# Kernel tuning notes

Measured on AMD Instinct MI355X. Metric: run time of the kernel, lower is better.

## Reference

```python
import jax, jax.numpy as jnp
import numpy as np

H = 0.5
EPS = 1e-08


def setup_inputs() -> dict:
    key = jax.random.key(0)
    k1, k2, k3 = jax.random.split(key, 3)
    B, in_dim, n_rules, out_dim = 16384, 64, 128, 32
    X = jax.random.normal(k1, (B, in_dim), dtype=jnp.float32)
    centers = jax.random.normal(k2, (in_dim, n_rules), dtype=jnp.float32)
    sigmas = jnp.ones((in_dim, n_rules), dtype=jnp.float32)
    W = jax.random.normal(k3, (out_dim, (in_dim + 1) * n_rules), dtype=jnp.float32) * 0.02
    b = jnp.zeros((out_dim,), dtype=jnp.float32)
    return {"X": X, "centers": centers, "sigmas": sigmas, "W": W, "b": b}


def reference(X, centers, sigmas, W, b):
    # HTSK firing levels: mean-style scaled Gaussian log-memberships summed over in_dim
    scale = H / sigmas ** 2 + EPS                      # [in_dim, n_rules]
    diff = X[:, :, None] - centers[None, :, :]          # [B, in_dim, n_rules]
    logits = jnp.sum(-(diff ** 2) * scale, axis=1)      # [B, n_rules]
    frs = jax.nn.softmax(logits, axis=1)                # [B, n_rules]
    B = X.shape[0]
    # order=1 consequent input: rule-major outer product, then raw firing levels
    xr = (frs[:, :, None] * X[:, None, :]).reshape(B, -1)  # [B, n_rules*in_dim]
    Z = jnp.concatenate([xr, frs], axis=1)               # [B, n_rules*(in_dim+1)]
    output = Z @ W.T + b                                 # [B, out_dim]
    return output, frs
```

## Files before the change

### kernel.cpp

```cpp
#include <hip/hip_runtime.h>


#define H_CONST 0.5f
#define EPS_CONST 1e-8f
#define NROWS 16384
#define NRULES 128
#define WCOLS 8320

typedef _Float16 half8 __attribute__((ext_vector_type(8)));
typedef float floatx4 __attribute__((ext_vector_type(4)));

#define MFMA16(a, b, c) __builtin_amdgcn_mfma_f32_16x16x32_f16((a), (b), (c), 0, 0, 0)

#define WFRAG_OFF 0
#define W0FRAG_OFF 262144
#define BMAT_OFF   (262144 + 4096)
#define KVEC_BYTE_OFF 630784
#define WS_BYTES_NEEDED (630784 + 512)

__global__ __launch_bounds__(256) void prep_kernel(
    const float* __restrict__ centers, const float* __restrict__ sigmas,
    const float* __restrict__ W, _Float16* __restrict__ wsh)
{
    __shared__ float sBuf[32 * 68];
    const int t = threadIdx.x;
    const int b = blockIdx.x;

    if (b < 128) {
        const int r = b;
        {
            int o = t >> 3, seg = t & 7;
            const float* g = W + o * WCOLS + r * 64 + seg * 8;
            floatx4 a = *(const floatx4*)g;
            floatx4 c = *(const floatx4*)(g + 4);
            *(floatx4*)(sBuf + o * 68 + seg * 8) = a;
            *(floatx4*)(sBuf + o * 68 + seg * 8 + 4) = c;
        }
        __syncthreads();
        {
            int L = t & 63, nt = (t >> 6) & 1, s = t >> 7;
            int o = nt * 16 + (L & 15);
            int ib = s * 32 + ((L >> 4) & 3) * 8;
            floatx4 fa = *(const floatx4*)(sBuf + o * 68 + ib);
            floatx4 fb = *(const floatx4*)(sBuf + o * 68 + ib + 4);
            half8 h;
#pragma unroll
            for (int k = 0; k < 8; ++k) h[k] = (_Float16)((k < 4) ? fa[k & 3] : fb[k & 3]);
            *(half8*)(wsh + WFRAG_OFF + r * 2048 + t * 8) = h;
        }
    } else if (b < 136) {
        const int nt = b - 128;
        float* sS = sBuf;
        float* sC = sBuf + 1088;
        {
            int i = t >> 2, c0 = (t & 3) * 4;
            floatx4 sg4 = *(const floatx4*)(sigmas + i * NRULES + nt * 16 + c0);
            floatx4 ct4 = *(const floatx4*)(centers + i * NRULES + nt * 16 + c0);
#pragma unroll
            for (int k = 0; k < 4; ++k) { sS[i * 17 + c0 + k] = sg4[k]; sC[i * 17 + c0 + k] = ct4[k]; }
        }
        __syncthreads();
#pragma unroll
        for (int kk = 0; kk < 3; ++kk) {
            int unit = t + kk * 256;
            int s = unit >> 6, L = unit & 63;
            int q = (L >> 4) & 3, nl = L & 15;
            int g = s >> 1;
            int i0 = (s & 1) * 32 + q * 8;
            half8 h;
#pragma unroll
            for (int j = 0; j < 8; ++j) {
                int i = i0 + j;
                float sg = sS[i * 17 + nl];
                float S = H_CONST / (sg * sg) + EPS_CONST;
                float c = sC[i * 17 + nl];
                float CS2 = 2.0f * c * S;
                _Float16 v;
                if (g == 0 || g == 2) v = -(_Float16)S;
                else if (g == 1) { _Float16 sh = (_Float16)S; v = -(_Float16)(S - (float)sh); }
                else if (g == 3 || g == 5) v = (_Float16)CS2;
                else { _Float16 ch = (_Float16)CS2; v = (_Float16)(CS2 - (float)ch); }
                h[j] = v;
            }
            *(half8*)(wsh + BMAT_OFF + ((s * 8 + nt) * 64 + L) * 8) = h;
        }
    } else {
#pragma unroll
        for (int kk = 0; kk < 2; ++kk) {
            int unit = t + kk * 256;
            int s = unit >> 7, nt = (unit >> 6) & 1, L = unit & 63;
            int q = (L >> 4) & 3;
            int o = nt * 16 + (L & 15);
            half8 h;
#pragma unroll
            for (int j = 0; j < 8; ++j) {
                int r = s * 32 + q * 8 + j;
                h[j] = (_Float16)W[o * WCOLS + 8192 + r];
            }
            *(half8*)(wsh + W0FRAG_OFF + ((s * 2 + nt) * 64 + L) * 8) = h;
        }
    }
}

__global__ __launch_bounds__(128) void prep_kvec(
    const float* __restrict__ centers, const float* __restrict__ sigmas,
    float* __restrict__ kvec)
{
    int r = threadIdx.x;
    float acc = 0.f;
#pragma unroll 8
    for (int i = 0; i < 64; ++i) {
        float sg = sigmas[i * NRULES + r];
        float S = H_CONST / (sg * sg) + EPS_CONST;
        float c = centers[i * NRULES + r];
        acc += c * c * S;
    }
    kvec[r] = acc;
}

__global__ __launch_bounds__(256) void main_fused(
    const float* __restrict__ X, const float* __restrict__ bias,
    const _Float16* __restrict__ wsh, const float* __restrict__ kvec,
    float* __restrict__ out, float* __restrict__ frs_out)
{
    __shared__ _Float16 sXh[32 * 64];
    __shared__ _Float16 sXl[32 * 64];
    __shared__ _Float16 sX2h[32 * 64];
    __shared__ _Float16 sX2l[32 * 64];
    __shared__ _Float16 sF[32 * 136];
    __shared__ float sU[4608];

    const int t = threadIdx.x;
    const int w = t >> 6;
    const int L = t & 63;
    const int m = L & 15;
    const int q = L >> 4;
    const int row0 = blockIdx.x * 32;

    {
        int row = t >> 3, uc = t & 7;
        const float* gx = X + (row0 + row) * 64 + uc * 8;
        floatx4 xa = *(const floatx4*)gx;
        floatx4 xb = *(const floatx4*)(gx + 4);
        int base = row * 64 + (uc ^ (row & 7)) * 8;
        half8 vh, vl, v2h, v2l;
#pragma unroll
        for (int k = 0; k < 8; ++k) {
            float x = (k < 4) ? xa[k & 3] : xb[k & 3];
            _Float16 xh = (_Float16)x;
            _Float16 xl2 = (_Float16)(x - (float)xh);
            float x2 = x * x;
            _Float16 x2h = (_Float16)x2;
            _Float16 x2l = (_Float16)(x2 - (float)x2h);
            vh[k] = xh; vl[k] = xl2; v2h[k] = x2h; v2l[k] = x2l;
        }
        *(half8*)(sXh + base) = vh;
        *(half8*)(sXl + base) = vl;
        *(half8*)(sX2h + base) = v2h;
        *(half8*)(sX2l + base) = v2l;
    }
    __syncthreads();

    floatx4 lacc[2][2];
#pragma unroll
    for (int mt = 0; mt < 2; ++mt)
#pragma unroll
        for (int n = 0; n < 2; ++n) lacc[mt][n] = (floatx4){0.f, 0.f, 0.f, 0.f};

    const _Float16* Bm = wsh + BMAT_OFF;
#pragma unroll
    for (int s = 0; s < 12; ++s) {
        const _Float16* arr = (s < 4) ? sX2h : (s < 6) ? sX2l : (s < 10) ? sXh : sXl;
        int phys = (((s & 1) << 2) | q) ^ (m & 7);
        half8 b0 = *(const half8*)(Bm + ((s * 8 + 2 * w + 0) * 64 + L) * 8);
        half8 b1 = *(const half8*)(Bm + ((s * 8 + 2 * w + 1) * 64 + L) * 8);
#pragma unroll
        for (int mt = 0; mt < 2; ++mt) {
            half8 a = *(const half8*)(arr + (mt * 16 + m) * 64 + phys * 8);
            lacc[mt][0] = MFMA16(a, b0, lacc[mt][0]);
            lacc[mt][1] = MFMA16(a, b1, lacc[mt][1]);
        }
    }
    float kv0 = kvec[(2 * w + 0) * 16 + m];
    float kv1 = kvec[(2 * w + 1) * 16 + m];

#pragma unroll
    for (int mt = 0; mt < 2; ++mt)
#pragma unroll
        for (int ntl = 0; ntl < 2; ++ntl)
#pragma unroll
            for (int reg = 0; reg < 4; ++reg) {
                int rl = mt * 16 + q * 4 + reg;
                int col = (2 * w + ntl) * 16 + m;
                sU[rl * 132 + col] = lacc[mt][ntl][reg] - (ntl ? kv1 : kv0);
            }
    __syncthreads();

    {
        int row = t >> 3, l8 = t & 7;
        int base = row * 132 + l8 * 16;
        float v[16];
        float mx = -1e30f;
#pragma unroll
        for (int k = 0; k < 16; ++k) { v[k] = sU[base + k]; mx = fmaxf(mx, v[k]); }
        mx = fmaxf(mx, __shfl_xor(mx, 1));
        mx = fmaxf(mx, __shfl_xor(mx, 2));
        mx = fmaxf(mx, __shfl_xor(mx, 4));
        float sum = 0.f;
#pragma unroll
        for (int k = 0; k < 16; ++k) { v[k] = __expf(v[k] - mx); sum += v[k]; }
        sum += __shfl_xor(sum, 1);
        sum += __shfl_xor(sum, 2);
        sum += __shfl_xor(sum, 4);
        float inv = 1.0f / sum;
        float* gf = frs_out + (row0 + row) * 128 + l8 * 16;
        half8 h0, h1;
#pragma unroll
        for (int c = 0; c < 4; ++c) {
            floatx4 o4;
#pragma unroll
            for (int k = 0; k < 4; ++k) {
                float f = v[c * 4 + k] * inv;
                o4[k] = f;
                if (c < 2) h0[c * 4 + k] = (_Float16)f; else h1[(c - 2) * 4 + k] = (_Float16)f;
            }
            *(floatx4*)(gf + c * 4) = o4;
        }
        *(half8*)(sF + row * 136 + l8 * 16) = h0;
        *(half8*)(sF + row * 136 + l8 * 16 + 8) = h1;
    }
    __syncthreads();

    const int rq = w;
    const int r0 = rq * 32;
    const _Float16* Wf = wsh + WFRAG_OFF;
    const _Float16* W0f = wsh + W0FRAG_OFF;

#define LDW(r, slot) (*(const half8*)(Wf + (r) * 2048 + ((slot) * 64 + L) * 8))

    half8 xf[2][2];
#pragma unroll
    for (int mt = 0; mt < 2; ++mt)
#pragma unroll
        for (int s = 0; s < 2; ++s) {
            int phys = ((s << 2) | q) ^ (m & 7);
            xf[mt][s] = *(const half8*)(sXh + (mt * 16 + m) * 64 + phys * 8);
        }

    floatx4 oacc[2][2];
#pragma unroll
    for (int mt = 0; mt < 2; ++mt)
#pragma unroll
        for (int n = 0; n < 2; ++n) oacc[mt][n] = (floatx4){0.f, 0.f, 0.f, 0.f};

    half8 b00 = LDW(r0, 0), b01 = LDW(r0, 1), b10 = LDW(r0, 2), b11 = LDW(r0, 3);

#pragma unroll
    for (int rg = 0; rg < 4; ++rg) {
        half8 fv0 = *(const half8*)(sF + (0 * 16 + m) * 136 + r0 + rg * 8);
        half8 fv1 = *(const half8*)(sF + (1 * 16 + m) * 136 + r0 + rg * 8);
#pragma unroll
        for (int rr2 = 0; rr2 < 8; ++rr2) {
            half8 c00 = b00, c01 = b01, c10 = b10, c11 = b11;
            if (rg * 8 + rr2 < 31) {
                int rn = r0 + rg * 8 + rr2 + 1;
                b00 = LDW(rn, 0); b01 = LDW(rn, 1); b10 = LDW(rn, 2); b11 = LDW(rn, 3);
            }
            _Float16 f0 = fv0[rr2], f1 = fv1[rr2];
            half8 fs0, fs1;
#pragma unroll
            for (int k = 0; k < 8; ++k) { fs0[k] = f0; fs1[k] = f1; }
            half8 a00 = fs0 * xf[0][0];
            half8 a01 = fs0 * xf[0][1];
            half8 a10 = fs1 * xf[1][0];
            half8 a11 = fs1 * xf[1][1];
            oacc[0][0] = MFMA16(a00, c00, oacc[0][0]);
            oacc[0][0] = MFMA16(a01, c10, oacc[0][0]);
            oacc[0][1] = MFMA16(a00, c01, oacc[0][1]);
            oacc[0][1] = MFMA16(a01, c11, oacc[0][1]);
            oacc[1][0] = MFMA16(a10, c00, oacc[1][0]);
            oacc[1][0] = MFMA16(a11, c10, oacc[1][0]);
            oacc[1][1] = MFMA16(a10, c01, oacc[1][1]);
            oacc[1][1] = MFMA16(a11, c11, oacc[1][1]);
        }
    }

    {
        half8 wb0 = *(const half8*)(W0f + ((rq * 2 + 0) * 64 + L) * 8);
        half8 wb1 = *(const half8*)(W0f + ((rq * 2 + 1) * 64 + L) * 8);
#pragma unroll
        for (int mt = 0; mt < 2; ++mt) {
            half8 a = *(const half8*)(sF + (mt * 16 + m) * 136 + rq * 32 + q * 8);
            oacc[mt][0] = MFMA16(a, wb0, oacc[mt][0]);
            oacc[mt][1] = MFMA16(a, wb1, oacc[mt][1]);
        }
    }

#pragma unroll
    for (int mt = 0; mt < 2; ++mt)
#pragma unroll
        for (int ntl = 0; ntl < 2; ++ntl)
#pragma unroll
            for (int reg = 0; reg < 4; ++reg)
                sU[w * 1152 + (mt * 16 + q * 4 + reg) * 36 + ntl * 16 + m] = oacc[mt][ntl][reg];
    __syncthreads();

    {
        int row = t >> 3, col0 = (t & 7) * 4;
        floatx4 acc = *(const floatx4*)(sU + 0 * 1152 + row * 36 + col0);
        acc += *(const floatx4*)(sU + 1 * 1152 + row * 36 + col0);
        acc += *(const floatx4*)(sU + 2 * 1152 + row * 36 + col0);
        acc += *(const floatx4*)(sU + 3 * 1152 + row * 36 + col0);
        acc += *(const floatx4*)(bias + col0);
        *(floatx4*)(out + (row0 + row) * 32 + col0) = acc;
    }
#undef LDW
}

extern "C" void kernel_launch(void* const* d_in, const int* in_sizes, int n_in,
                              void* d_out, int out_size, void* d_ws, size_t ws_size,
                              hipStream_t stream) {
    const float* X = (const float*)d_in[0];
    const float* centers = (const float*)d_in[1];
    const float* sigmas = (const float*)d_in[2];
    const float* W = (const float*)d_in[3];
    const float* b = (const float*)d_in[4];
    float* outp = (float*)d_out;
    float* frs_out = outp + NROWS * 32;
    if (ws_size < (size_t)WS_BYTES_NEEDED) return;
    _Float16* wsh = (_Float16*)d_ws;
    float* kvec = (float*)((char*)d_ws + KVEC_BYTE_OFF);

    prep_kernel<<<137, 256, 0, stream>>>(centers, sigmas, W, wsh);
    prep_kvec<<<1, 128, 0, stream>>>(centers, sigmas, kvec);
    main_fused<<<NROWS / 32, 256, 0, stream>>>(X, b, wsh, kvec, outp, frs_out);
}
```

Baseline: 91.04 us.

## Merge kvec prep into prep kernel and prefetch weight fragments earlier

```diff
diff --git a/kernel.cpp b/kernel.cpp
--- a/kernel.cpp
+++ b/kernel.cpp
@@ -20,7 +20,7 @@
 
 __global__ __launch_bounds__(256) void prep_kernel(
     const float* __restrict__ centers, const float* __restrict__ sigmas,
-    const float* __restrict__ W, _Float16* __restrict__ wsh)
+    const float* __restrict__ W, _Float16* __restrict__ wsh, float* __restrict__ kvec)
 {
     __shared__ float sBuf[32 * 68];
     const int t = threadIdx.x;
@@ -99,23 +99,19 @@
             }
             *(half8*)(wsh + W0FRAG_OFF + ((s * 2 + nt) * 64 + L) * 8) = h;
         }
-    }
-}
-
-__global__ __launch_bounds__(128) void prep_kvec(
-    const float* __restrict__ centers, const float* __restrict__ sigmas,
-    float* __restrict__ kvec)
-{
-    int r = threadIdx.x;
-    float acc = 0.f;
+        if (t < 128) {
+            int r = t;
+            float acc = 0.f;
 #pragma unroll 8
-    for (int i = 0; i < 64; ++i) {
-        float sg = sigmas[i * NRULES + r];
-        float S = H_CONST / (sg * sg) + EPS_CONST;
-        float c = centers[i * NRULES + r];
-        acc += c * c * S;
-    }
-    kvec[r] = acc;
+            for (int i = 0; i < 64; ++i) {
+                float sg = sigmas[i * NRULES + r];
+                float S = H_CONST / (sg * sg) + EPS_CONST;
+                float c = centers[i * NRULES + r];
+                acc += c * c * S;
+            }
+            kvec[r] = acc;
+        }
+    }
 }
 
 __global__ __launch_bounds__(256) void main_fused(
@@ -137,6 +133,16 @@
     const int q = L >> 4;
     const int row0 = blockIdx.x * 32;
 
+    const _Float16* Bm = wsh + BMAT_OFF;
+    half8 Bv[12][2];
+#pragma unroll
+    for (int s = 0; s < 12; ++s) {
+        Bv[s][0] = *(const half8*)(Bm + ((s * 8 + 2 * w + 0) * 64 + L) * 8);
+        Bv[s][1] = *(const half8*)(Bm + ((s * 8 + 2 * w + 1) * 64 + L) * 8);
+    }
+    float kv0 = kvec[(2 * w + 0) * 16 + m];
+    float kv1 = kvec[(2 * w + 1) * 16 + m];
+
     {
         int row = t >> 3, uc = t & 7;
         const float* gx = X + (row0 + row) * 64 + uc * 8;
@@ -167,22 +173,17 @@
 #pragma unroll
         for (int n = 0; n < 2; ++n) lacc[mt][n] = (floatx4){0.f, 0.f, 0.f, 0.f};
 
-    const _Float16* Bm = wsh + BMAT_OFF;
 #pragma unroll
     for (int s = 0; s < 12; ++s) {
         const _Float16* arr = (s < 4) ? sX2h : (s < 6) ? sX2l : (s < 10) ? sXh : sXl;
         int phys = (((s & 1) << 2) | q) ^ (m & 7);
-        half8 b0 = *(const half8*)(Bm + ((s * 8 + 2 * w + 0) * 64 + L) * 8);
-        half8 b1 = *(const half8*)(Bm + ((s * 8 + 2 * w + 1) * 64 + L) * 8);
 #pragma unroll
         for (int mt = 0; mt < 2; ++mt) {
             half8 a = *(const half8*)(arr + (mt * 16 + m) * 64 + phys * 8);
-            lacc[mt][0] = MFMA16(a, b0, lacc[mt][0]);
-            lacc[mt][1] = MFMA16(a, b1, lacc[mt][1]);
-        }
-    }
-    float kv0 = kvec[(2 * w + 0) * 16 + m];
-    float kv1 = kvec[(2 * w + 1) * 16 + m];
+            lacc[mt][0] = MFMA16(a, Bv[s][0], lacc[mt][0]);
+            lacc[mt][1] = MFMA16(a, Bv[s][1], lacc[mt][1]);
+        }
+    }
 
 #pragma unroll
     for (int mt = 0; mt < 2; ++mt)
@@ -194,6 +195,24 @@
                 int col = (2 * w + ntl) * 16 + m;
                 sU[rl * 132 + col] = lacc[mt][ntl][reg] - (ntl ? kv1 : kv0);
             }
+
+    const int rq = w;
+    const int r0 = rq * 32;
+    const _Float16* Wf = wsh + WFRAG_OFF;
+    const _Float16* W0f = wsh + W0FRAG_OFF;
+#define LDW(r, slot) (*(const half8*)(Wf + (r) * 2048 + ((slot) * 64 + L) * 8))
+
+    half8 ring[4][4];
+#pragma unroll
+    for (int p = 0; p < 4; ++p) {
+        ring[p][0] = LDW(r0 + p, 0);
+        ring[p][1] = LDW(r0 + p, 1);
+        ring[p][2] = LDW(r0 + p, 2);
+        ring[p][3] = LDW(r0 + p, 3);
+    }
+    half8 wb0 = *(const half8*)(W0f + ((rq * 2 + 0) * 64 + L) * 8);
+    half8 wb1 = *(const half8*)(W0f + ((rq * 2 + 1) * 64 + L) * 8);
+
     __syncthreads();
 
     {
@@ -231,13 +250,6 @@
     }
     __syncthreads();
 
-    const int rq = w;
-    const int r0 = rq * 32;
-    const _Float16* Wf = wsh + WFRAG_OFF;
-    const _Float16* W0f = wsh + W0FRAG_OFF;
-
-#define LDW(r, slot) (*(const half8*)(Wf + (r) * 2048 + ((slot) * 64 + L) * 8))
-
     half8 xf[2][2];
 #pragma unroll
     for (int mt = 0; mt < 2; ++mt)
@@ -253,18 +265,22 @@
 #pragma unroll
         for (int n = 0; n < 2; ++n) oacc[mt][n] = (floatx4){0.f, 0.f, 0.f, 0.f};
 
-    half8 b00 = LDW(r0, 0), b01 = LDW(r0, 1), b10 = LDW(r0, 2), b11 = LDW(r0, 3);
-
 #pragma unroll
     for (int rg = 0; rg < 4; ++rg) {
         half8 fv0 = *(const half8*)(sF + (0 * 16 + m) * 136 + r0 + rg * 8);
         half8 fv1 = *(const half8*)(sF + (1 * 16 + m) * 136 + r0 + rg * 8);
 #pragma unroll
         for (int rr2 = 0; rr2 < 8; ++rr2) {
-            half8 c00 = b00, c01 = b01, c10 = b10, c11 = b11;
-            if (rg * 8 + rr2 < 31) {
-                int rn = r0 + rg * 8 + rr2 + 1;
-                b00 = LDW(rn, 0); b01 = LDW(rn, 1); b10 = LDW(rn, 2); b11 = LDW(rn, 3);
+            int rr = rg * 8 + rr2;
+            int slot = rr & 3;
+            half8 c00 = ring[slot][0], c01 = ring[slot][1];
+            half8 c10 = ring[slot][2], c11 = ring[slot][3];
+            if (rr < 28) {
+                int rn = r0 + rr + 4;
+                ring[slot][0] = LDW(rn, 0);
+                ring[slot][1] = LDW(rn, 1);
+                ring[slot][2] = LDW(rn, 2);
+                ring[slot][3] = LDW(rn, 3);
             }
             _Float16 f0 = fv0[rr2], f1 = fv1[rr2];
             half8 fs0, fs1;
@@ -286,8 +302,6 @@
     }
 
     {
-        half8 wb0 = *(const half8*)(W0f + ((rq * 2 + 0) * 64 + L) * 8);
-        half8 wb1 = *(const half8*)(W0f + ((rq * 2 + 1) * 64 + L) * 8);
 #pragma unroll
         for (int mt = 0; mt < 2; ++mt) {
             half8 a = *(const half8*)(sF + (mt * 16 + m) * 136 + rq * 32 + q * 8);
@@ -331,7 +345,6 @@
     _Float16* wsh = (_Float16*)d_ws;
     float* kvec = (float*)((char*)d_ws + KVEC_BYTE_OFF);
 
-    prep_kernel<<<137, 256, 0, stream>>>(centers, sigmas, W, wsh);
-    prep_kvec<<<1, 128, 0, stream>>>(centers, sigmas, kvec);
+    prep_kernel<<<137, 256, 0, stream>>>(centers, sigmas, W, wsh, kvec);
     main_fused<<<NROWS / 32, 256, 0, stream>>>(X, b, wsh, kvec, outp, frs_out);
 }
```

Result: faster. 84.81 us (-6.8%).
